# Performance work log

Measured on AMD Instinct MI355X. Metric: run time of the kernel, lower is better.

The kernel has to match this reference:

```python
import jax, jax.numpy as jnp
import numpy as np

H, K_CHUNKS = 16, 16          # z_num = (h, k)
Z_DIM = 64
OC, IC, KW = 128, 128, 3      # per-chunk out, in, kernel width
HID = 256
O, I = H * OC, K_CHUNKS * IC  # 2048, 2048
L = 3
N_PDE, D_PDE = 1024, 64


def setup_inputs() -> dict:
    key = jax.random.key(0)
    ks = jax.random.split(key, 10)
    def rn(k, shape, scale=1.0):
        return jax.random.normal(k, shape, dtype=jnp.float32) * scale
    return {
        "Z": rn(ks[0], (H * K_CHUNKS, Z_DIM)),                 # stacked z_list (fmod(randn,2) ~ randn)
        "z_bias": rn(ks[1], (O,)),
        "unet_1d_weights": rn(ks[2], (O, I, L), 0.02),
        "unet_1d_bias": rn(ks[3], (O,), 0.02),
        "pde_inputs": rn(ks[4], (N_PDE, D_PDE)),
        "W1": rn(ks[5], (Z_DIM, HID), 1.0 / np.sqrt(Z_DIM)),
        "U1": rn(ks[6], (D_PDE, HID), 1.0 / np.sqrt(D_PDE)),
        "b1": jnp.zeros((HID,), jnp.float32),
        "W2": rn(ks[7], (HID, OC * IC * KW), 1.0 / np.sqrt(HID)),
        "b2": jnp.zeros((OC * IC * KW,), jnp.float32),
    }


def reference(Z, z_bias, unet_1d_weights, unet_1d_bias, pde_inputs, W1, U1, b1, W2, b2):
    # Batched hypernet: replaces the h*k sequential hyper_net calls.
    pde_feat = pde_inputs.mean(axis=0) @ U1                    # [HID], shared conditioning
    hidden = jnp.tanh(Z @ W1 + pde_feat + b1)                  # [h*k, HID]
    w = (hidden @ W2 + b2).reshape(H, K_CHUNKS, OC, IC, KW)    # per-chunk weights
    # cat over j along dim=1 (in-channels), then over i along dim=0 (out-channels)
    exe_unet_weight = w.transpose(0, 2, 1, 3, 4).reshape(O, I, KW)  # [O, I, K]
    w_2d = jnp.einsum('oik,oil->oikl', exe_unet_weight, unet_1d_weights)  # [O, I, K, L]
    bb = z_bias + unet_1d_bias                                 # [O]
    return (w_2d, bb)
```

## Files before the change

kernel.cpp:

```cpp
#include <hip/hip_runtime.h>
#include <hip/hip_bf16.h>
#include <math.h>

#define H_ 16
#define KC_ 16
#define ZD_ 64
#define HID_ 256
#define O_ 2048
#define NW2_ 49152
#define W2D_OUT 37748736
#define DPDE_ 64

typedef short bf16x8 __attribute__((ext_vector_type(8)));
typedef float f32x4 __attribute__((ext_vector_type(4)));

struct F3 { float x, y, z; };

static __device__ __forceinline__ unsigned short f2bf(float f) {
    union { float f; unsigned u; } v; v.f = f;
    unsigned r = v.u + 0x7FFF + ((v.u >> 16) & 1);
    return (unsigned short)(r >> 16);
}

__global__ void prep_kernel(const float* __restrict__ Z,
                            const float* __restrict__ pde,
                            const float* __restrict__ W1,
                            const float* __restrict__ U1,
                            const float* __restrict__ b1,
                            const float* __restrict__ z_bias,
                            const float* __restrict__ u_bias,
                            unsigned short* __restrict__ hiddenA,
                            float* __restrict__ out_bb) {
    __shared__ float part[16][64];
    __shared__ float meanv[64];
    __shared__ float zr[64];
    const int t = threadIdx.x, m = blockIdx.x;
    if (t < 64) zr[t] = Z[m * ZD_ + t];
    const int c4 = t & 15, rg = t >> 4;
    float sx = 0.f, sy = 0.f, sz = 0.f, sw = 0.f;
    const float4* p = (const float4*)pde;
    for (int r = 0; r < 64; ++r) {
        float4 v = p[(rg * 64 + r) * 16 + c4];
        sx += v.x; sy += v.y; sz += v.z; sw += v.w;
    }
    part[rg][c4 * 4 + 0] = sx; part[rg][c4 * 4 + 1] = sy;
    part[rg][c4 * 4 + 2] = sz; part[rg][c4 * 4 + 3] = sw;
    __syncthreads();
    if (t < 64) {
        float a = 0.f;
        #pragma unroll
        for (int g = 0; g < 16; ++g) a += part[g][t];
        meanv[t] = a * (1.f / 1024.f);
    }
    __syncthreads();
    float f = b1[t];
    #pragma unroll
    for (int d = 0; d < 64; ++d) f = fmaf(meanv[d], U1[d * HID_ + t], f);
    float s = f;
    #pragma unroll
    for (int d = 0; d < 64; ++d) s = fmaf(zr[d], W1[d * HID_ + t], s);
    hiddenA[((size_t)(t >> 3) * 256 + m) * 8 + (t & 7)] = f2bf(tanhf(s));
    if (m < 8) {
        const int idx = m * 256 + t;
        out_bb[idx] = z_bias[idx] + u_bias[idx];
    }
}

__global__ __launch_bounds__(512, 4)
void gemm_expand(const unsigned short* __restrict__ hiddenA,
                 const float* __restrict__ W2,
                 const float* __restrict__ b2,
                 const float* __restrict__ unet,
                 float* __restrict__ out) {
    __shared__ unsigned short bT[96 * 72];

    const int t = threadIdx.x;
    const int lane = t & 63;
    const int wave = t >> 6;
    const int n15 = lane & 15;
    const int quad = lane >> 4;
    const int oc = blockIdx.x >> 2;
    const int icq = blockIdx.x & 3;
    const int n0g = oc * 384 + icq * 96;

    f32x4 acc[2][6];
    #pragma unroll
    for (int a = 0; a < 2; ++a)
        #pragma unroll
        for (int b = 0; b < 6; ++b) acc[a][b] = (f32x4){0.f, 0.f, 0.f, 0.f};

    for (int c = 0; c < 4; ++c) {
        #pragma unroll
        for (int i = 0; i < 3; ++i) {
            const int e = i * 512 + t;
            const int kk = e / 24;
            const int nq = e - kk * 24;
            const float4 v = *(const float4*)(W2 + (size_t)(c * 64 + kk) * NW2_ + n0g + nq * 4);
            unsigned short* d = &bT[(nq * 4) * 72 + kk];
            d[0]       = f2bf(v.x);
            d[72]      = f2bf(v.y);
            d[144]     = f2bf(v.z);
            d[216]     = f2bf(v.w);
        }
        __syncthreads();
        #pragma unroll
        for (int kh = 0; kh < 2; ++kh) {
            const int g = c * 8 + kh * 4 + quad;
            bf16x8 afr[2];
            #pragma unroll
            for (int mi = 0; mi < 2; ++mi)
                afr[mi] = *(const bf16x8*)(hiddenA +
                          ((size_t)g * 256 + (wave * 2 + mi) * 16 + n15) * 8);
            #pragma unroll
            for (int nt = 0; nt < 6; ++nt) {
                const bf16x8 bfr = *(const bf16x8*)&bT[(nt * 16 + n15) * 72 + kh * 32 + quad * 8];
                acc[0][nt] = __builtin_amdgcn_mfma_f32_16x16x32_bf16(afr[0], bfr, acc[0][nt], 0, 0, 0);
                acc[1][nt] = __builtin_amdgcn_mfma_f32_16x16x32_bf16(afr[1], bfr, acc[1][nt], 0, 0, 0);
            }
        }
        __syncthreads();
    }

    #pragma unroll
    for (int mi = 0; mi < 2; ++mi) {
        const int o = (wave * 2 + mi) * 128 + oc;
        const float* ub_o = unet + (size_t)o * 6144;
        float* ob_o = out + (size_t)o * 18432;
        #pragma unroll
        for (int nt = 0; nt < 6; ++nt) {
            const int nl = nt * 16 + n15;
            const int n_rel = icq * 96 + nl;
            const int ic = n_rel / 3;
            const float gb2 = b2[n0g + nl];
            #pragma unroll
            for (int r = 0; r < 4; ++r) {
                const int kc = quad * 4 + r;
                const float w = acc[mi][nt][r] + gb2;
                const F3 u = *(const F3*)(ub_o + kc * 384 + ic * 3);
                F3 res; res.x = w * u.x; res.y = w * u.y; res.z = w * u.z;
                *(F3*)(ob_o + kc * 1152 + n_rel * 3) = res;
            }
        }
    }
}

extern "C" void kernel_launch(void* const* d_in, const int* in_sizes, int n_in,
                              void* d_out, int out_size, void* d_ws, size_t ws_size,
                              hipStream_t stream) {
    const float* Z       = (const float*)d_in[0];
    const float* z_bias  = (const float*)d_in[1];
    const float* unet_w  = (const float*)d_in[2];
    const float* unet_b  = (const float*)d_in[3];
    const float* pde     = (const float*)d_in[4];
    const float* W1      = (const float*)d_in[5];
    const float* U1      = (const float*)d_in[6];
    const float* b1      = (const float*)d_in[7];
    const float* W2      = (const float*)d_in[8];
    const float* b2      = (const float*)d_in[9];
    float* out = (float*)d_out;

    unsigned short* hiddenA = (unsigned short*)d_ws;

    prep_kernel<<<256, 256, 0, stream>>>(Z, pde, W1, U1, b1, z_bias, unet_b,
                                         hiddenA, out + W2D_OUT);
    gemm_expand<<<512, 512, 0, stream>>>(hiddenA, W2, b2, unet_w, out);
}
```

Before: 277.9 us.

## Stage full W2 K-range in LDS once with packed bf16 pairs and swizzle

```diff
diff --git a/kernel.cpp b/kernel.cpp
--- a/kernel.cpp
+++ b/kernel.cpp
@@ -20,6 +20,10 @@
     union { float f; unsigned u; } v; v.f = f;
     unsigned r = v.u + 0x7FFF + ((v.u >> 16) & 1);
     return (unsigned short)(r >> 16);
+}
+
+static __device__ __forceinline__ unsigned pack2(float lo, float hi) {
+    return (unsigned)f2bf(lo) | ((unsigned)f2bf(hi) << 16);
 }
 
 __global__ void prep_kernel(const float* __restrict__ Z,
@@ -66,13 +70,15 @@
     }
 }
 
+#define BT_S2 132
+
 __global__ __launch_bounds__(512, 4)
 void gemm_expand(const unsigned short* __restrict__ hiddenA,
                  const float* __restrict__ W2,
                  const float* __restrict__ b2,
                  const float* __restrict__ unet,
                  float* __restrict__ out) {
-    __shared__ unsigned short bT[96 * 72];
+    __shared__ unsigned bT[96 * BT_S2];
 
     const int t = threadIdx.x;
     const int lane = t & 63;
@@ -83,42 +89,50 @@
     const int icq = blockIdx.x & 3;
     const int n0g = oc * 384 + icq * 96;
 
+    #pragma unroll
+    for (int i = 0; i < 6; ++i) {
+        const int u  = i * 512 + t;
+        const int kp = u / 24;
+        const int nq = u - kp * 24;
+        const float* p0 = W2 + (size_t)(2 * kp) * NW2_ + n0g + nq * 4;
+        const float4 va = *(const float4*)p0;
+        const float4 vb = *(const float4*)(p0 + NW2_);
+        const int kpx = kp ^ ((nq & 7) << 1) ^ (((nq >> 3) & 1) << 4);
+        unsigned* r0 = &bT[(4 * nq) * BT_S2 + kpx];
+        r0[0 * BT_S2] = pack2(va.x, vb.x);
+        r0[1 * BT_S2] = pack2(va.y, vb.y);
+        r0[2 * BT_S2] = pack2(va.z, vb.z);
+        r0[3 * BT_S2] = pack2(va.w, vb.w);
+    }
+    __syncthreads();
+
     f32x4 acc[2][6];
     #pragma unroll
     for (int a = 0; a < 2; ++a)
         #pragma unroll
         for (int b = 0; b < 6; ++b) acc[a][b] = (f32x4){0.f, 0.f, 0.f, 0.f};
 
-    for (int c = 0; c < 4; ++c) {
+    #pragma unroll
+    for (int ks = 0; ks < 8; ++ks) {
+        const int g = ks * 4 + quad;
+        bf16x8 afr[2];
         #pragma unroll
-        for (int i = 0; i < 3; ++i) {
-            const int e = i * 512 + t;
-            const int kk = e / 24;
-            const int nq = e - kk * 24;
-            const float4 v = *(const float4*)(W2 + (size_t)(c * 64 + kk) * NW2_ + n0g + nq * 4);
-            unsigned short* d = &bT[(nq * 4) * 72 + kk];
-            d[0]       = f2bf(v.x);
-            d[72]      = f2bf(v.y);
-            d[144]     = f2bf(v.z);
-            d[216]     = f2bf(v.w);
+        for (int mi = 0; mi < 2; ++mi)
+            afr[mi] = *(const bf16x8*)(hiddenA +
+                      ((size_t)g * 256 + (wave * 2 + mi) * 16 + n15) * 8);
+        const int base4 = ks * 16 + quad * 4;
+        #pragma unroll
+        for (int nt = 0; nt < 6; ++nt) {
+            const int n = nt * 16 + n15;
+            const int nqr = n >> 2;
+            const int swz = ((nqr & 7) << 1) ^ (((nqr >> 3) & 1) << 4);
+            const unsigned* row = &bT[n * BT_S2];
+            union { bf16x8 v; unsigned long long q[2]; } bb;
+            bb.q[0] = *(const unsigned long long*)&row[(base4)     ^ swz];
+            bb.q[1] = *(const unsigned long long*)&row[(base4 + 2) ^ swz];
+            acc[0][nt] = __builtin_amdgcn_mfma_f32_16x16x32_bf16(afr[0], bb.v, acc[0][nt], 0, 0, 0);
+            acc[1][nt] = __builtin_amdgcn_mfma_f32_16x16x32_bf16(afr[1], bb.v, acc[1][nt], 0, 0, 0);
         }
-        __syncthreads();
-        #pragma unroll
-        for (int kh = 0; kh < 2; ++kh) {
-            const int g = c * 8 + kh * 4 + quad;
-            bf16x8 afr[2];
-            #pragma unroll
-            for (int mi = 0; mi < 2; ++mi)
-                afr[mi] = *(const bf16x8*)(hiddenA +
-                          ((size_t)g * 256 + (wave * 2 + mi) * 16 + n15) * 8);
-            #pragma unroll
-            for (int nt = 0; nt < 6; ++nt) {
-                const bf16x8 bfr = *(const bf16x8*)&bT[(nt * 16 + n15) * 72 + kh * 32 + quad * 8];
-                acc[0][nt] = __builtin_amdgcn_mfma_f32_16x16x32_bf16(afr[0], bfr, acc[0][nt], 0, 0, 0);
-                acc[1][nt] = __builtin_amdgcn_mfma_f32_16x16x32_bf16(afr[1], bfr, acc[1][nt], 0, 0, 0);
-            }
-        }
-        __syncthreads();
     }
 
     #pragma unroll
```

Result: no change. 280.2 us (+0.8%).
